# Optimization experiments

Measured on AMD Instinct MI355X. Metric: run time of the kernel, lower is better.

## Reference

```python
import jax, jax.numpy as jnp
import numpy as np

N_NODES = 50000
N_EDGES = 800000
IN_CH = 256
HID = 32
HEADS = 8
OUT_CH = 64
NEG_SLOPE = 0.2


def _glorot(key, shape):
    fan = shape[0] + shape[-1]
    lim = jnp.sqrt(6.0 / fan)
    return jax.random.uniform(key, shape, jnp.float32, -lim, lim)


def setup_inputs() -> dict:
    key = jax.random.key(0)
    ks = jax.random.split(key, 12)
    x = jax.random.normal(ks[0], (N_NODES, IN_CH), jnp.float32)
    edge_index = jax.random.randint(ks[1], (2, N_EDGES), 0, N_NODES, jnp.int64 if jax.config.jax_enable_x64 else jnp.int32)
    # conv1: in -> heads*hid, concat
    W1 = _glorot(ks[2], (IN_CH, HEADS * HID))
    a_src1 = _glorot(ks[3], (HEADS, HID))
    a_dst1 = _glorot(ks[4], (HEADS, HID))
    b1 = jnp.zeros((HEADS * HID,), jnp.float32)
    # conv2: heads*hid -> heads*hid, 1 head
    W2 = _glorot(ks[5], (HEADS * HID, HEADS * HID))
    a_src2 = _glorot(ks[6], (1, HEADS * HID))
    a_dst2 = _glorot(ks[7], (1, HEADS * HID))
    b2 = jnp.zeros((HEADS * HID,), jnp.float32)
    # final linear
    Wlin = _glorot(ks[8], (HEADS * HID, OUT_CH))
    blin = jnp.zeros((OUT_CH,), jnp.float32)
    return {"x": x, "edge_index": edge_index, "W1": W1, "a_src1": a_src1,
            "a_dst1": a_dst1, "b1": b1, "W2": W2, "a_src2": a_src2,
            "a_dst2": a_dst2, "b2": b2, "Wlin": Wlin, "blin": blin}


def gat_conv(x, src, dst, W, a_src, a_dst, bias, heads, out_ch):
    n = x.shape[0]
    h = (x @ W).reshape(n, heads, out_ch)            # [N, H, C]
    # per-node attention halves, then gather per edge (cheaper than edge-first)
    s = jnp.einsum('nhc,hc->nh', h, a_src)[src]      # [E, H]
    d = jnp.einsum('nhc,hc->nh', h, a_dst)[dst]      # [E, H]
    e = jax.nn.leaky_relu(s + d, NEG_SLOPE)          # [E, H]
    # segment softmax over incoming edges of each dst node
    emax = jax.ops.segment_max(e, dst, num_segments=n)
    e = jnp.exp(e - jax.lax.stop_gradient(emax)[dst])
    denom = jax.ops.segment_sum(e, dst, num_segments=n)
    alpha = e / denom[dst]                           # [E, H]
    msg = h[src] * alpha[:, :, None]                 # [E, H, C]
    out = jax.ops.segment_sum(msg, dst, num_segments=n)
    return out.reshape(n, heads * out_ch) + bias


def reference(x, edge_index, W1, a_src1, a_dst1, b1, W2, a_src2, a_dst2, b2, Wlin, blin):
    n = x.shape[0]
    # PyG GATConv adds self-loops by default
    loops = jnp.arange(n, dtype=edge_index.dtype)
    src = jnp.concatenate([edge_index[0], loops])
    dst = jnp.concatenate([edge_index[1], loops])
    # dropout (p=0.6) is identity in eval mode
    h = jax.nn.elu(gat_conv(x, src, dst, W1, a_src1, a_dst1, b1, HEADS, HID))
    h = jax.nn.elu(gat_conv(h, src, dst, W2, a_src2, a_dst2, b2, 1, HEADS * HID))
    return h @ Wlin + blin
```

## Files before the change

### kernel.cpp

```cpp
#include <hip/hip_runtime.h>
#include <hip/hip_bf16.h>
#include <hip/hip_fp16.h>

typedef __attribute__((ext_vector_type(8))) short short8;
typedef __attribute__((ext_vector_type(4))) float f32x4;

#define GLL(g, s) __builtin_amdgcn_global_load_lds(                        \
    (const __attribute__((address_space(1))) void*)(g),                    \
    (__attribute__((address_space(3))) void*)(s), 16, 0, 0)

__device__ __forceinline__ ushort f2bf(float f) {
    unsigned u = __float_as_uint(f);
    u += 0x7fffu + ((u >> 16) & 1u);
    return (ushort)(u >> 16);
}
__device__ __forceinline__ float bf2f(ushort h) {
    return __uint_as_float(((unsigned)h) << 16);
}
__device__ __forceinline__ float elu_f(float x) {
    return x > 0.0f ? x : expm1f(x);
}
__device__ __forceinline__ float lrelu(float x) {
    return x < 0.0f ? 0.2f * x : x;
}

__global__ void hist_kernel(const int* __restrict__ ei, int* __restrict__ deg, int E, int n) {
    int total = E + n;
    for (int i = blockIdx.x * blockDim.x + threadIdx.x; i < total; i += gridDim.x * blockDim.x) {
        int d = (i < E) ? ei[E + i] : (i - E);
        atomicAdd(&deg[d], 1);
    }
}

__global__ __launch_bounds__(256) void partial_kernel(const int* __restrict__ deg, int* __restrict__ bsums, int n) {
    __shared__ int sm[256];
    int t = threadIdx.x;
    int idx = blockIdx.x * 256 + t;
    sm[t] = (idx < n) ? deg[idx] : 0;
    __syncthreads();
    #pragma unroll
    for (int off = 128; off > 0; off >>= 1) {
        if (t < off) sm[t] += sm[t + off];
        __syncthreads();
    }
    if (t == 0) bsums[blockIdx.x] = sm[0];
}

__global__ __launch_bounds__(256) void scanblocks_kernel(const int* __restrict__ bsums, int* __restrict__ boff,
                                                         int* __restrict__ rowptr, int nb, int n) {
    __shared__ int sm[256];
    int t = threadIdx.x;
    int carry = 0;
    for (int base = 0; base < nb; base += 256) {
        int i = base + t;
        int v = (i < nb) ? bsums[i] : 0;
        sm[t] = v;
        __syncthreads();
        #pragma unroll
        for (int off = 1; off < 256; off <<= 1) {
            int x = (t >= off) ? sm[t - off] : 0;
            __syncthreads();
            sm[t] += x;
            __syncthreads();
        }
        if (i < nb) boff[i] = carry + sm[t] - v;
        int tot = sm[255];
        __syncthreads();
        carry += tot;
    }
    if (t == 0) rowptr[n] = carry;
}

__global__ __launch_bounds__(256) void finalize_kernel(const int* __restrict__ deg, const int* __restrict__ boff,
                                                       int* __restrict__ rowptr, int* __restrict__ cursor, int n) {
    __shared__ int sm[256];
    int t = threadIdx.x;
    int idx = blockIdx.x * 256 + t;
    int v = (idx < n) ? deg[idx] : 0;
    sm[t] = v;
    __syncthreads();
    #pragma unroll
    for (int off = 1; off < 256; off <<= 1) {
        int x = (t >= off) ? sm[t - off] : 0;
        __syncthreads();
        sm[t] += x;
        __syncthreads();
    }
    if (idx < n) {
        int ex = boff[blockIdx.x] + sm[t] - v;
        rowptr[idx] = ex;
        cursor[idx] = ex;
    }
}

__global__ void scatter_kernel(const int* __restrict__ ei, int* __restrict__ cursor,
                               int* __restrict__ csr_src, int E, int n) {
    int total = E + n;
    for (int i = blockIdx.x * blockDim.x + threadIdx.x; i < total; i += gridDim.x * blockDim.x) {
        int s, d;
        if (i < E) { s = ei[i]; d = ei[E + i]; }
        else       { s = i - E; d = s; }
        int pos = atomicAdd(&cursor[d], 1);
        csr_src[pos] = s;
    }
}

__global__ void wconv_kernel(const float* __restrict__ W, short* __restrict__ hi,
                             short* __restrict__ lo, int KN, int Ncols) {
    int idx = blockIdx.x * 256 + threadIdx.x;
    if (idx >= KN) return;
    int k = idx / Ncols, n = idx - k * Ncols;
    float v = W[idx];
    ushort h = f2bf(v);
    ushort l = f2bf(v - bf2f(h));
    size_t o = ((size_t)(k >> 3) * Ncols + n) * 8 + (k & 7);
    hi[o] = (short)h;
    lo[o] = (short)l;
}

template<int N, bool OUTHALF>
__global__ __launch_bounds__(256, 2) void gemm_mfma(const float* __restrict__ A,
                                                    const short* __restrict__ Bph,
                                                    const short* __restrict__ Bpl,
                                                    const float* __restrict__ bias,
                                                    void* __restrict__ Cout, int M) {
    constexpr int FN = (N == 256) ? 4 : 1;
    __shared__ short Bh[4][2][4][64][8];
    __shared__ short Bl[4][2][4][64][8];
    const int tid = threadIdx.x;
    const int lane = tid & 63;
    const int wave = tid >> 6;
    const int r0 = blockIdx.x * 64;
    const int c = lane >> 4;
    const int rs = lane & 15;
    const int c0 = (N == 256) ? wave * 64 : 0;
    const int colin = (N == 256) ? rs : (wave * 16 + rs);

    const float* aBase[4];
    #pragma unroll
    for (int fm = 0; fm < 4; ++fm) {
        int r = r0 + fm * 16 + rs;
        if (r > M - 1) r = M - 1;
        aBase[fm] = A + (size_t)r * 256 + c * 8;
    }

    float4 aregA[8], aregB[8];
    auto loadA = [&](float4* ar, int t) {
        #pragma unroll
        for (int fm = 0; fm < 4; ++fm) {
            ar[2 * fm]     = *(const float4*)(aBase[fm] + t * 32);
            ar[2 * fm + 1] = *(const float4*)(aBase[fm] + t * 32 + 4);
        }
    };
    auto issueB = [&](int buf, int t) {
        #pragma unroll
        for (int q = 0; q < 4; ++q) {
            const short* sh = Bph + ((size_t)(t * 4 + q) * N + c0 + lane) * 8;
            const short* sl = Bpl + ((size_t)(t * 4 + q) * N + c0 + lane) * 8;
            GLL(sh, &Bh[wave][buf][q][0][0]);
            GLL(sl, &Bl[wave][buf][q][0][0]);
        }
    };
    auto convA = [&](const float4* ar, short8* ah, short8* al) {
        #pragma unroll
        for (int fm = 0; fm < 4; ++fm) {
            float f[8] = {ar[2 * fm].x, ar[2 * fm].y, ar[2 * fm].z, ar[2 * fm].w,
                          ar[2 * fm + 1].x, ar[2 * fm + 1].y, ar[2 * fm + 1].z, ar[2 * fm + 1].w};
            short8 hi, lo;
            #pragma unroll
            for (int j = 0; j < 8; ++j) {
                ushort hb = f2bf(f[j]);
                hi[j] = (short)hb;
                lo[j] = (short)f2bf(f[j] - bf2f(hb));
            }
            ah[fm] = hi;
            al[fm] = lo;
        }
    };

    f32x4 acc[4][FN];
    #pragma unroll
    for (int i = 0; i < 4; ++i)
        #pragma unroll
        for (int j = 0; j < FN; ++j)
            acc[i][j] = (f32x4){0.f, 0.f, 0.f, 0.f};

    loadA(aregA, 0); issueB(0, 0);
    loadA(aregB, 1); issueB(1, 1);

    #pragma unroll
    for (int t = 0; t < 8; ++t) {
        if (t < 7) asm volatile("s_waitcnt vmcnt(16)" ::: "memory");
        else       asm volatile("s_waitcnt vmcnt(0)" ::: "memory");
        const int cur = t & 1;
        const float4* curA = (t & 1) ? aregB : aregA;
        short8 ah[4], al[4];
        convA(curA, ah, al);
        #pragma unroll
        for (int fn = 0; fn < FN; ++fn) {
            short8 bhv = *(const short8*)&Bh[wave][cur][c][colin + fn * 16][0];
            short8 blv = *(const short8*)&Bl[wave][cur][c][colin + fn * 16][0];
            #pragma unroll
            for (int fm = 0; fm < 4; ++fm) {
                acc[fm][fn] = __builtin_amdgcn_mfma_f32_16x16x32_bf16(ah[fm], bhv, acc[fm][fn], 0, 0, 0);
                acc[fm][fn] = __builtin_amdgcn_mfma_f32_16x16x32_bf16(ah[fm], blv, acc[fm][fn], 0, 0, 0);
                acc[fm][fn] = __builtin_amdgcn_mfma_f32_16x16x32_bf16(al[fm], bhv, acc[fm][fn], 0, 0, 0);
            }
        }
        asm volatile("s_waitcnt lgkmcnt(0)" ::: "memory");
        if (t < 6) {
            float4* nxtA = (t & 1) ? aregB : aregA;
            loadA(nxtA, t + 2);
            issueB(cur, t + 2);
        }
    }

    const int wn0 = wave * (N / 4);
    #pragma unroll
    for (int fn = 0; fn < FN; ++fn) {
        int col = wn0 + fn * 16 + rs;
        float bv = bias ? bias[col] : 0.0f;
        #pragma unroll
        for (int fm = 0; fm < 4; ++fm) {
            #pragma unroll
            for (int g = 0; g < 4; ++g) {
                int r = r0 + fm * 16 + c * 4 + g;
                if (r < M) {
                    float v = acc[fm][fn][g] + bv;
                    if constexpr (OUTHALF)
                        ((__half*)Cout)[(size_t)r * N + col] = __float2half_rn(v);
                    else
                        ((float*)Cout)[(size_t)r * N + col] = v;
                }
            }
        }
    }
}

template<int HEADS>
__global__ __launch_bounds__(256) void sd_kernel(const __half* __restrict__ h, const float* __restrict__ a_src,
                                                 const float* __restrict__ a_dst, float* __restrict__ s_out,
                                                 float* __restrict__ d_out_, int nnodes) {
    int lane = threadIdx.x & 63;
    int node = blockIdx.x * 4 + (threadIdx.x >> 6);
    if (node >= nnodes) return;
    const __half2* hp = (const __half2*)(h + (size_t)node * 256 + lane * 4);
    float2 f01 = __half22float2(hp[0]);
    float2 f23 = __half22float2(hp[1]);
    float4 as = *(const float4*)&a_src[lane * 4];
    float4 ad = *(const float4*)&a_dst[lane * 4];
    float ps = f01.x * as.x + f01.y * as.y + f23.x * as.z + f23.y * as.w;
    float pd = f01.x * ad.x + f01.y * ad.y + f23.x * ad.z + f23.y * ad.w;
    const int GS = 64 / HEADS;
    #pragma unroll
    for (int off = 1; off < GS; off <<= 1) {
        ps += __shfl_xor(ps, off);
        pd += __shfl_xor(pd, off);
    }
    int g = lane / GS;
    int r = lane & (GS - 1);
    if (r == 0) s_out[(size_t)node * HEADS + g] = ps;
    if (r == 1) d_out_[(size_t)node * HEADS + g] = pd;
}

template<int HEADS>
__global__ __launch_bounds__(256) void agg_kernel(const int* __restrict__ rowptr, const int* __restrict__ csr_src,
                                                  const __half* __restrict__ h, const float* __restrict__ s_att,
                                                  const float* __restrict__ d_att, const float* __restrict__ bias,
                                                  float* __restrict__ out, int nnodes) {
    int lane = threadIdx.x & 63;
    int node = blockIdx.x * 4 + (threadIdx.x >> 6);
    if (node >= nnodes) return;
    const int hh = (HEADS == 8) ? (lane >> 3) : 0;
    const int cbase = lane * 4;
    const int begin = rowptr[node], end = rowptr[node + 1];
    const float dl = d_att[(size_t)node * HEADS + hh];
    float m = -1e30f, den = 0.f;
    float ax = 0.f, ay = 0.f, az = 0.f, aw = 0.f;
    int i = begin;
    for (; i + 4 <= end; i += 4) {
        int s0 = csr_src[i], s1 = csr_src[i + 1], s2 = csr_src[i + 2], s3 = csr_src[i + 3];
        uint2 u0 = *(const uint2*)(h + (size_t)s0 * 256 + cbase);
        uint2 u1 = *(const uint2*)(h + (size_t)s1 * 256 + cbase);
        uint2 u2 = *(const uint2*)(h + (size_t)s2 * 256 + cbase);
        uint2 u3 = *(const uint2*)(h + (size_t)s3 * 256 + cbase);
        float v0 = lrelu(s_att[(size_t)s0 * HEADS + hh] + dl);
        float v1 = lrelu(s_att[(size_t)s1 * HEADS + hh] + dl);
        float v2 = lrelu(s_att[(size_t)s2 * HEADS + hh] + dl);
        float v3 = lrelu(s_att[(size_t)s3 * HEADS + hh] + dl);
        float vb = fmaxf(fmaxf(v0, v1), fmaxf(v2, v3));
        float mn = fmaxf(m, vb);
        float sc = __expf(m - mn);
        float w0 = __expf(v0 - mn), w1 = __expf(v1 - mn);
        float w2 = __expf(v2 - mn), w3 = __expf(v3 - mn);
        m = mn;
        den = den * sc + (w0 + w1) + (w2 + w3);
        float2 f0a = __half22float2(*(const __half2*)&u0.x), f0b = __half22float2(*(const __half2*)&u0.y);
        float2 f1a = __half22float2(*(const __half2*)&u1.x), f1b = __half22float2(*(const __half2*)&u1.y);
        float2 f2a = __half22float2(*(const __half2*)&u2.x), f2b = __half22float2(*(const __half2*)&u2.y);
        float2 f3a = __half22float2(*(const __half2*)&u3.x), f3b = __half22float2(*(const __half2*)&u3.y);
        ax = ax * sc + w0 * f0a.x + w1 * f1a.x + w2 * f2a.x + w3 * f3a.x;
        ay = ay * sc + w0 * f0a.y + w1 * f1a.y + w2 * f2a.y + w3 * f3a.y;
        az = az * sc + w0 * f0b.x + w1 * f1b.x + w2 * f2b.x + w3 * f3b.x;
        aw = aw * sc + w0 * f0b.y + w1 * f1b.y + w2 * f2b.y + w3 * f3b.y;
    }
    for (; i < end; ++i) {
        int s0 = csr_src[i];
        uint2 u0 = *(const uint2*)(h + (size_t)s0 * 256 + cbase);
        float v0 = lrelu(s_att[(size_t)s0 * HEADS + hh] + dl);
        float mn = fmaxf(m, v0);
        float sc = __expf(m - mn);
        float w0 = __expf(v0 - mn);
        m = mn;
        den = den * sc + w0;
        float2 f0a = __half22float2(*(const __half2*)&u0.x), f0b = __half22float2(*(const __half2*)&u0.y);
        ax = ax * sc + w0 * f0a.x;
        ay = ay * sc + w0 * f0a.y;
        az = az * sc + w0 * f0b.x;
        aw = aw * sc + w0 * f0b.y;
    }
    float inv = 1.0f / den;
    float4 bv = *(const float4*)&bias[cbase];
    float4 r;
    r.x = elu_f(ax * inv + bv.x);
    r.y = elu_f(ay * inv + bv.y);
    r.z = elu_f(az * inv + bv.z);
    r.w = elu_f(aw * inv + bv.w);
    *(float4*)&out[(size_t)node * 256 + cbase] = r;
}

extern "C" void kernel_launch(void* const* d_in, const int* in_sizes, int n_in,
                              void* d_out, int out_size, void* d_ws, size_t ws_size,
                              hipStream_t stream) {
    const float* x      = (const float*)d_in[0];
    const int*   ei     = (const int*)d_in[1];
    const float* W1     = (const float*)d_in[2];
    const float* a_src1 = (const float*)d_in[3];
    const float* a_dst1 = (const float*)d_in[4];
    const float* b1     = (const float*)d_in[5];
    const float* W2     = (const float*)d_in[6];
    const float* a_src2 = (const float*)d_in[7];
    const float* a_dst2 = (const float*)d_in[8];
    const float* b2     = (const float*)d_in[9];
    const float* Wlin   = (const float*)d_in[10];
    const float* blin   = (const float*)d_in[11];
    float* out = (float*)d_out;

    const int N = in_sizes[0] / 256;
    const int E = in_sizes[1] / 2;
    const int ET = E + N;
    const int NB = (N + 255) / 256;

    char* p = (char*)d_ws;
    auto alloc = [&](size_t bytes) {
        void* r = (void*)p;
        p += (bytes + 255) & ~size_t(255);
        return r;
    };
    __half* bufH  = (__half*)alloc((size_t)N * 256 * 2);
    float* bufB   = (float*)alloc((size_t)N * 256 * 4);
    float* s1     = (float*)alloc((size_t)N * 8 * 4);
    float* d1     = (float*)alloc((size_t)N * 8 * 4);
    float* s2     = (float*)alloc((size_t)N * 4);
    float* d2     = (float*)alloc((size_t)N * 4);
    int*   deg    = (int*)alloc((size_t)N * 4);
    int*   cursor = (int*)alloc((size_t)N * 4);
    int*   rowptr = (int*)alloc((size_t)(N + 1) * 4);
    int*   csr    = (int*)alloc((size_t)ET * 4);
    int*   bsums  = (int*)alloc((size_t)NB * 4);
    int*   boff   = (int*)alloc((size_t)NB * 4);
    short* W1h    = (short*)alloc((size_t)256 * 256 * 2);
    short* W1l    = (short*)alloc((size_t)256 * 256 * 2);
    short* W2h    = (short*)alloc((size_t)256 * 256 * 2);
    short* W2l    = (short*)alloc((size_t)256 * 256 * 2);
    short* W3h    = (short*)alloc((size_t)256 * 64 * 2);
    short* W3l    = (short*)alloc((size_t)256 * 64 * 2);

    hipMemsetAsync(deg, 0, (size_t)N * 4, stream);
    hist_kernel<<<(ET + 255) / 256, 256, 0, stream>>>(ei, deg, E, N);
    partial_kernel<<<NB, 256, 0, stream>>>(deg, bsums, N);
    scanblocks_kernel<<<1, 256, 0, stream>>>(bsums, boff, rowptr, NB, N);
    finalize_kernel<<<NB, 256, 0, stream>>>(deg, boff, rowptr, cursor, N);
    scatter_kernel<<<(ET + 255) / 256, 256, 0, stream>>>(ei, cursor, csr, E, N);

    wconv_kernel<<<(256 * 256 + 255) / 256, 256, 0, stream>>>(W1, W1h, W1l, 256 * 256, 256);
    wconv_kernel<<<(256 * 256 + 255) / 256, 256, 0, stream>>>(W2, W2h, W2l, 256 * 256, 256);
    wconv_kernel<<<(256 * 64 + 255) / 256, 256, 0, stream>>>(Wlin, W3h, W3l, 256 * 64, 64);

    const int gBlocks = (N + 63) / 64;
    const int nodeBlocks = (N + 3) / 4;

    gemm_mfma<256, true><<<gBlocks, 256, 0, stream>>>(x, W1h, W1l, nullptr, bufH, N);
    sd_kernel<8><<<nodeBlocks, 256, 0, stream>>>(bufH, a_src1, a_dst1, s1, d1, N);
    agg_kernel<8><<<nodeBlocks, 256, 0, stream>>>(rowptr, csr, bufH, s1, d1, b1, bufB, N);

    gemm_mfma<256, true><<<gBlocks, 256, 0, stream>>>(bufB, W2h, W2l, nullptr, bufH, N);
    sd_kernel<1><<<nodeBlocks, 256, 0, stream>>>(bufH, a_src2, a_dst2, s2, d2, N);
    agg_kernel<1><<<nodeBlocks, 256, 0, stream>>>(rowptr, csr, bufH, s2, d2, b2, bufB, N);

    gemm_mfma<64, false><<<gBlocks, 256, 0, stream>>>(bufB, W3h, W3l, blin, out, N);
}
```

Baseline: 517.4 us.

## Pre-pack activations to split-bf16, single-wave GEMMs, fixed-offset softmax, fused scan

The split-bf16 conversion of x moves into a single packing kernel, and the aggregation kernels now write their outputs straight into a k-major hi/lo bf16 layout. The GEMMs can then load A via global_load_lds instead of converting fp32 in registers. The GEMM becomes a 64-thread block with a 2D grid, and the scan's block-offset pass is merged into the finalize kernel. The aggregation drops the online-max softmax in favour of exp2 with a fixed offset of 30, which removes the rescaling work but risks overflow or underflow for attention logits far from that offset.

New measurement: 577.5 us. 11.6% more time.

```diff
diff --git a/kernel.cpp b/kernel.cpp
--- a/kernel.cpp
+++ b/kernel.cpp
@@ -46,36 +46,26 @@
     if (t == 0) bsums[blockIdx.x] = sm[0];
 }
 
-__global__ __launch_bounds__(256) void scanblocks_kernel(const int* __restrict__ bsums, int* __restrict__ boff,
-                                                         int* __restrict__ rowptr, int nb, int n) {
+__global__ __launch_bounds__(256) void finalize2_kernel(const int* __restrict__ deg, const int* __restrict__ bsums,
+                                                        int* __restrict__ rowptr, int* __restrict__ cursor,
+                                                        int n, int nb) {
     __shared__ int sm[256];
-    int t = threadIdx.x;
-    int carry = 0;
-    for (int base = 0; base < nb; base += 256) {
-        int i = base + t;
-        int v = (i < nb) ? bsums[i] : 0;
-        sm[t] = v;
+    __shared__ int sbase;
+    int t = threadIdx.x, b = blockIdx.x;
+    int part = 0;
+    for (int i = t; i < b; i += 256) part += bsums[i];
+    sm[t] = part;
+    __syncthreads();
+    #pragma unroll
+    for (int off = 128; off > 0; off >>= 1) {
+        if (t < off) sm[t] += sm[t + off];
         __syncthreads();
-        #pragma unroll
-        for (int off = 1; off < 256; off <<= 1) {
-            int x = (t >= off) ? sm[t - off] : 0;
-            __syncthreads();
-            sm[t] += x;
-            __syncthreads();
-        }
-        if (i < nb) boff[i] = carry + sm[t] - v;
-        int tot = sm[255];
-        __syncthreads();
-        carry += tot;
-    }
-    if (t == 0) rowptr[n] = carry;
-}
-
-__global__ __launch_bounds__(256) void finalize_kernel(const int* __restrict__ deg, const int* __restrict__ boff,
-                                                       int* __restrict__ rowptr, int* __restrict__ cursor, int n) {
-    __shared__ int sm[256];
-    int t = threadIdx.x;
-    int idx = blockIdx.x * 256 + t;
+    }
+    if (t == 0) sbase = sm[0];
+    __syncthreads();
+    int base = sbase;
+    __syncthreads();
+    int idx = b * 256 + t;
     int v = (idx < n) ? deg[idx] : 0;
     sm[t] = v;
     __syncthreads();
@@ -87,10 +77,11 @@
         __syncthreads();
     }
     if (idx < n) {
-        int ex = boff[blockIdx.x] + sm[t] - v;
+        int ex = base + sm[t] - v;
         rowptr[idx] = ex;
         cursor[idx] = ex;
     }
+    if (b == nb - 1 && t == 255) rowptr[n] = base + sm[255];
 }
 
 __global__ void scatter_kernel(const int* __restrict__ ei, int* __restrict__ cursor,
@@ -105,76 +96,73 @@
     }
 }
 
-__global__ void wconv_kernel(const float* __restrict__ W, short* __restrict__ hi,
-                             short* __restrict__ lo, int KN, int Ncols) {
-    int idx = blockIdx.x * 256 + threadIdx.x;
-    if (idx >= KN) return;
+__global__ __launch_bounds__(256) void packall_kernel(const float* __restrict__ x,
+                                                      const float* __restrict__ W1,
+                                                      const float* __restrict__ W2,
+                                                      const float* __restrict__ W3,
+                                                      short* __restrict__ xh, short* __restrict__ xl,
+                                                      short* __restrict__ w1h, short* __restrict__ w1l,
+                                                      short* __restrict__ w2h, short* __restrict__ w2l,
+                                                      short* __restrict__ w3h, short* __restrict__ w3l,
+                                                      int M, int Mpad, int XB) {
+    int b = blockIdx.x;
+    int t = threadIdx.x;
+    if (b < XB) {
+        int r = b * 8 + (t >> 5);
+        int cc = t & 31;
+        if (r >= M) return;
+        const float* src = x + (size_t)r * 256 + cc * 8;
+        short8 hi, lo;
+        #pragma unroll
+        for (int j = 0; j < 8; ++j) {
+            float v = src[j];
+            ushort h = f2bf(v);
+            hi[j] = (short)h;
+            lo[j] = (short)f2bf(v - bf2f(h));
+        }
+        size_t o = ((size_t)cc * Mpad + r) * 8;
+        *(short8*)(xh + o) = hi;
+        *(short8*)(xl + o) = lo;
+        return;
+    }
+    const float* W; short* hh; short* ll; int Ncols; int base;
+    if (b < XB + 256)      { W = W1; hh = w1h; ll = w1l; Ncols = 256; base = XB; }
+    else if (b < XB + 512) { W = W2; hh = w2h; ll = w2l; Ncols = 256; base = XB + 256; }
+    else                   { W = W3; hh = w3h; ll = w3l; Ncols = 64;  base = XB + 512; }
+    int idx = (b - base) * 256 + t;
     int k = idx / Ncols, n = idx - k * Ncols;
     float v = W[idx];
     ushort h = f2bf(v);
     ushort l = f2bf(v - bf2f(h));
     size_t o = ((size_t)(k >> 3) * Ncols + n) * 8 + (k & 7);
-    hi[o] = (short)h;
-    lo[o] = (short)l;
-}
-
-template<int N, bool OUTHALF>
-__global__ __launch_bounds__(256, 2) void gemm_mfma(const float* __restrict__ A,
-                                                    const short* __restrict__ Bph,
-                                                    const short* __restrict__ Bpl,
-                                                    const float* __restrict__ bias,
-                                                    void* __restrict__ Cout, int M) {
-    constexpr int FN = (N == 256) ? 4 : 1;
-    __shared__ short Bh[4][2][4][64][8];
-    __shared__ short Bl[4][2][4][64][8];
-    const int tid = threadIdx.x;
-    const int lane = tid & 63;
-    const int wave = tid >> 6;
+    hh[o] = (short)h;
+    ll[o] = (short)l;
+}
+
+template<int FN, bool OUTHALF>
+__global__ __launch_bounds__(64) void gemm_pk(const short* __restrict__ Aph, const short* __restrict__ Apl,
+                                              const short* __restrict__ Bph, const short* __restrict__ Bpl,
+                                              const float* __restrict__ bias, void* __restrict__ Cout,
+                                              int M, int Mpad, int NCOLS) {
+    __shared__ short Ah[2][4][64][8], Al[2][4][64][8];
+    __shared__ short Bh[2][4][FN * 16][8], Bl[2][4][FN * 16][8];
+    const int lane = threadIdx.x;
     const int r0 = blockIdx.x * 64;
+    const int c0 = blockIdx.y * FN * 16;
     const int c = lane >> 4;
     const int rs = lane & 15;
-    const int c0 = (N == 256) ? wave * 64 : 0;
-    const int colin = (N == 256) ? rs : (wave * 16 + rs);
-
-    const float* aBase[4];
-    #pragma unroll
-    for (int fm = 0; fm < 4; ++fm) {
-        int r = r0 + fm * 16 + rs;
-        if (r > M - 1) r = M - 1;
-        aBase[fm] = A + (size_t)r * 256 + c * 8;
-    }
-
-    float4 aregA[8], aregB[8];
-    auto loadA = [&](float4* ar, int t) {
-        #pragma unroll
-        for (int fm = 0; fm < 4; ++fm) {
-            ar[2 * fm]     = *(const float4*)(aBase[fm] + t * 32);
-            ar[2 * fm + 1] = *(const float4*)(aBase[fm] + t * 32 + 4);
-        }
-    };
-    auto issueB = [&](int buf, int t) {
+
+    auto issue = [&](int buf, int t) {
         #pragma unroll
         for (int q = 0; q < 4; ++q) {
-            const short* sh = Bph + ((size_t)(t * 4 + q) * N + c0 + lane) * 8;
-            const short* sl = Bpl + ((size_t)(t * 4 + q) * N + c0 + lane) * 8;
-            GLL(sh, &Bh[wave][buf][q][0][0]);
-            GLL(sl, &Bl[wave][buf][q][0][0]);
-        }
-    };
-    auto convA = [&](const float4* ar, short8* ah, short8* al) {
-        #pragma unroll
-        for (int fm = 0; fm < 4; ++fm) {
-            float f[8] = {ar[2 * fm].x, ar[2 * fm].y, ar[2 * fm].z, ar[2 * fm].w,
-                          ar[2 * fm + 1].x, ar[2 * fm + 1].y, ar[2 * fm + 1].z, ar[2 * fm + 1].w};
-            short8 hi, lo;
+            int kc = t * 4 + q;
+            GLL(Aph + ((size_t)kc * Mpad + r0 + lane) * 8, &Ah[buf][q][0][0]);
+            GLL(Apl + ((size_t)kc * Mpad + r0 + lane) * 8, &Al[buf][q][0][0]);
             #pragma unroll
-            for (int j = 0; j < 8; ++j) {
-                ushort hb = f2bf(f[j]);
-                hi[j] = (short)hb;
-                lo[j] = (short)f2bf(f[j] - bf2f(hb));
+            for (int hseg = 0; hseg < FN / 4; ++hseg) {
+                GLL(Bph + ((size_t)kc * NCOLS + c0 + hseg * 64 + lane) * 8, &Bh[buf][q][hseg * 64][0]);
+                GLL(Bpl + ((size_t)kc * NCOLS + c0 + hseg * 64 + lane) * 8, &Bl[buf][q][hseg * 64][0]);
             }
-            ah[fm] = hi;
-            al[fm] = lo;
         }
     };
 
@@ -185,40 +173,48 @@
         for (int j = 0; j < FN; ++j)
             acc[i][j] = (f32x4){0.f, 0.f, 0.f, 0.f};
 
-    loadA(aregA, 0); issueB(0, 0);
-    loadA(aregB, 1); issueB(1, 1);
+    issue(0, 0);
+    issue(1, 1);
 
     #pragma unroll
     for (int t = 0; t < 8; ++t) {
-        if (t < 7) asm volatile("s_waitcnt vmcnt(16)" ::: "memory");
-        else       asm volatile("s_waitcnt vmcnt(0)" ::: "memory");
-        const int cur = t & 1;
-        const float4* curA = (t & 1) ? aregB : aregA;
+        if (t < 7) {
+            if constexpr (FN == 8) asm volatile("s_waitcnt vmcnt(24)" ::: "memory");
+            else                   asm volatile("s_waitcnt vmcnt(16)" ::: "memory");
+        } else {
+            asm volatile("s_waitcnt vmcnt(0)" ::: "memory");
+        }
+        __builtin_amdgcn_sched_barrier(0);
+        const int buf = t & 1;
         short8 ah[4], al[4];
-        convA(curA, ah, al);
+        #pragma unroll
+        for (int fm = 0; fm < 4; ++fm) {
+            ah[fm] = *(const short8*)&Ah[buf][c][fm * 16 + rs][0];
+            al[fm] = *(const short8*)&Al[buf][c][fm * 16 + rs][0];
+        }
+        short8 bh[FN], bl[FN];
         #pragma unroll
         for (int fn = 0; fn < FN; ++fn) {
-            short8 bhv = *(const short8*)&Bh[wave][cur][c][colin + fn * 16][0];
-            short8 blv = *(const short8*)&Bl[wave][cur][c][colin + fn * 16][0];
+            bh[fn] = *(const short8*)&Bh[buf][c][fn * 16 + rs][0];
+            bl[fn] = *(const short8*)&Bl[buf][c][fn * 16 + rs][0];
+        }
+        asm volatile("s_waitcnt lgkmcnt(0)" ::: "memory");
+        __builtin_amdgcn_sched_barrier(0);
+        if (t < 6) issue(buf, t + 2);
+        #pragma unroll
+        for (int fn = 0; fn < FN; ++fn) {
             #pragma unroll
             for (int fm = 0; fm < 4; ++fm) {
-                acc[fm][fn] = __builtin_amdgcn_mfma_f32_16x16x32_bf16(ah[fm], bhv, acc[fm][fn], 0, 0, 0);
-                acc[fm][fn] = __builtin_amdgcn_mfma_f32_16x16x32_bf16(ah[fm], blv, acc[fm][fn], 0, 0, 0);
-                acc[fm][fn] = __builtin_amdgcn_mfma_f32_16x16x32_bf16(al[fm], bhv, acc[fm][fn], 0, 0, 0);
+                acc[fm][fn] = __builtin_amdgcn_mfma_f32_16x16x32_bf16(ah[fm], bh[fn], acc[fm][fn], 0, 0, 0);
+                acc[fm][fn] = __builtin_amdgcn_mfma_f32_16x16x32_bf16(ah[fm], bl[fn], acc[fm][fn], 0, 0, 0);
+                acc[fm][fn] = __builtin_amdgcn_mfma_f32_16x16x32_bf16(al[fm], bh[fn], acc[fm][fn], 0, 0, 0);
             }
         }
-        asm volatile("s_waitcnt lgkmcnt(0)" ::: "memory");
-        if (t < 6) {
-            float4* nxtA = (t & 1) ? aregB : aregA;
-            loadA(nxtA, t + 2);
-            issueB(cur, t + 2);
-        }
-    }
-
-    const int wn0 = wave * (N / 4);
+    }
+
     #pragma unroll
     for (int fn = 0; fn < FN; ++fn) {
-        int col = wn0 + fn * 16 + rs;
+        int col = c0 + fn * 16 + rs;
         float bv = bias ? bias[col] : 0.0f;
         #pragma unroll
         for (int fm = 0; fm < 4; ++fm) {
@@ -228,9 +224,9 @@
                 if (r < M) {
                     float v = acc[fm][fn][g] + bv;
                     if constexpr (OUTHALF)
-                        ((__half*)Cout)[(size_t)r * N + col] = __float2half_rn(v);
+                        ((__half*)Cout)[(size_t)r * NCOLS + col] = __float2half_rn(v);
                     else
-                        ((float*)Cout)[(size_t)r * N + col] = v;
+                        ((float*)Cout)[(size_t)r * NCOLS + col] = v;
                 }
             }
         }
@@ -259,15 +255,16 @@
     }
     int g = lane / GS;
     int r = lane & (GS - 1);
-    if (r == 0) s_out[(size_t)node * HEADS + g] = ps;
-    if (r == 1) d_out_[(size_t)node * HEADS + g] = pd;
+    if (r == 0) s_out[(size_t)node * HEADS + g] = ps * 1.44269504f;
+    if (r == 1) d_out_[(size_t)node * HEADS + g] = pd * 1.44269504f;
 }
 
 template<int HEADS>
 __global__ __launch_bounds__(256) void agg_kernel(const int* __restrict__ rowptr, const int* __restrict__ csr_src,
                                                   const __half* __restrict__ h, const float* __restrict__ s_att,
                                                   const float* __restrict__ d_att, const float* __restrict__ bias,
-                                                  float* __restrict__ out, int nnodes) {
+                                                  short* __restrict__ outh, short* __restrict__ outl,
+                                                  int nnodes, int Mpad) {
     int lane = threadIdx.x & 63;
     int node = blockIdx.x * 4 + (threadIdx.x >> 6);
     if (node >= nnodes) return;
@@ -275,7 +272,7 @@
     const int cbase = lane * 4;
     const int begin = rowptr[node], end = rowptr[node + 1];
     const float dl = d_att[(size_t)node * HEADS + hh];
-    float m = -1e30f, den = 0.f;
+    float den = 0.f;
     float ax = 0.f, ay = 0.f, az = 0.f, aw = 0.f;
     int i = begin;
     for (; i + 4 <= end; i += 4) {
@@ -284,49 +281,48 @@
         uint2 u1 = *(const uint2*)(h + (size_t)s1 * 256 + cbase);
         uint2 u2 = *(const uint2*)(h + (size_t)s2 * 256 + cbase);
         uint2 u3 = *(const uint2*)(h + (size_t)s3 * 256 + cbase);
-        float v0 = lrelu(s_att[(size_t)s0 * HEADS + hh] + dl);
-        float v1 = lrelu(s_att[(size_t)s1 * HEADS + hh] + dl);
-        float v2 = lrelu(s_att[(size_t)s2 * HEADS + hh] + dl);
-        float v3 = lrelu(s_att[(size_t)s3 * HEADS + hh] + dl);
-        float vb = fmaxf(fmaxf(v0, v1), fmaxf(v2, v3));
-        float mn = fmaxf(m, vb);
-        float sc = __expf(m - mn);
-        float w0 = __expf(v0 - mn), w1 = __expf(v1 - mn);
-        float w2 = __expf(v2 - mn), w3 = __expf(v3 - mn);
-        m = mn;
-        den = den * sc + (w0 + w1) + (w2 + w3);
+        float w0 = exp2f(lrelu(s_att[(size_t)s0 * HEADS + hh] + dl) - 30.0f);
+        float w1 = exp2f(lrelu(s_att[(size_t)s1 * HEADS + hh] + dl) - 30.0f);
+        float w2 = exp2f(lrelu(s_att[(size_t)s2 * HEADS + hh] + dl) - 30.0f);
+        float w3 = exp2f(lrelu(s_att[(size_t)s3 * HEADS + hh] + dl) - 30.0f);
+        den += (w0 + w1) + (w2 + w3);
         float2 f0a = __half22float2(*(const __half2*)&u0.x), f0b = __half22float2(*(const __half2*)&u0.y);
         float2 f1a = __half22float2(*(const __half2*)&u1.x), f1b = __half22float2(*(const __half2*)&u1.y);
         float2 f2a = __half22float2(*(const __half2*)&u2.x), f2b = __half22float2(*(const __half2*)&u2.y);
         float2 f3a = __half22float2(*(const __half2*)&u3.x), f3b = __half22float2(*(const __half2*)&u3.y);
-        ax = ax * sc + w0 * f0a.x + w1 * f1a.x + w2 * f2a.x + w3 * f3a.x;
-        ay = ay * sc + w0 * f0a.y + w1 * f1a.y + w2 * f2a.y + w3 * f3a.y;
-        az = az * sc + w0 * f0b.x + w1 * f1b.x + w2 * f2b.x + w3 * f3b.x;
-        aw = aw * sc + w0 * f0b.y + w1 * f1b.y + w2 * f2b.y + w3 * f3b.y;
+        ax += w0 * f0a.x + w1 * f1a.x + w2 * f2a.x + w3 * f3a.x;
+        ay += w0 * f0a.y + w1 * f1a.y + w2 * f2a.y + w3 * f3a.y;
+        az += w0 * f0b.x + w1 * f1b.x + w2 * f2b.x + w3 * f3b.x;
+        aw += w0 * f0b.y + w1 * f1b.y + w2 * f2b.y + w3 * f3b.y;
     }
     for (; i < end; ++i) {
         int s0 = csr_src[i];
         uint2 u0 = *(const uint2*)(h + (size_t)s0 * 256 + cbase);
-        float v0 = lrelu(s_att[(size_t)s0 * HEADS + hh] + dl);
-        float mn = fmaxf(m, v0);
-        float sc = __expf(m - mn);
-        float w0 = __expf(v0 - mn);
-        m = mn;
-        den = den * sc + w0;
+        float w0 = exp2f(lrelu(s_att[(size_t)s0 * HEADS + hh] + dl) - 30.0f);
+        den += w0;
         float2 f0a = __half22float2(*(const __half2*)&u0.x), f0b = __half22float2(*(const __half2*)&u0.y);
-        ax = ax * sc + w0 * f0a.x;
-        ay = ay * sc + w0 * f0a.y;
-        az = az * sc + w0 * f0b.x;
-        aw = aw * sc + w0 * f0b.y;
+        ax += w0 * f0a.x;
+        ay += w0 * f0a.y;
+        az += w0 * f0b.x;
+        aw += w0 * f0b.y;
     }
     float inv = 1.0f / den;
     float4 bv = *(const float4*)&bias[cbase];
-    float4 r;
-    r.x = elu_f(ax * inv + bv.x);
-    r.y = elu_f(ay * inv + bv.y);
-    r.z = elu_f(az * inv + bv.z);
-    r.w = elu_f(aw * inv + bv.w);
-    *(float4*)&out[(size_t)node * 256 + cbase] = r;
+    float r0 = elu_f(ax * inv + bv.x);
+    float r1 = elu_f(ay * inv + bv.y);
+    float r2 = elu_f(az * inv + bv.z);
+    float r3 = elu_f(aw * inv + bv.w);
+    ushort h0 = f2bf(r0), h1 = f2bf(r1), h2 = f2bf(r2), h3 = f2bf(r3);
+    ushort l0 = f2bf(r0 - bf2f(h0)), l1 = f2bf(r1 - bf2f(h1));
+    ushort l2 = f2bf(r2 - bf2f(h2)), l3 = f2bf(r3 - bf2f(h3));
+    size_t o = ((size_t)(lane >> 1) * Mpad + node) * 8 + (lane & 1) * 4;
+    uint2 hv, lv;
+    hv.x = (unsigned)h0 | ((unsigned)h1 << 16);
+    hv.y = (unsigned)h2 | ((unsigned)h3 << 16);
+    lv.x = (unsigned)l0 | ((unsigned)l1 << 16);
+    lv.y = (unsigned)l2 | ((unsigned)l3 << 16);
+    *(uint2*)(outh + o) = hv;
+    *(uint2*)(outl + o) = lv;
 }
 
 extern "C" void kernel_launch(void* const* d_in, const int* in_sizes, int n_in,
@@ -350,6 +346,7 @@
     const int E = in_sizes[1] / 2;
     const int ET = E + N;
     const int NB = (N + 255) / 256;
+    const int Mpad = ((N + 63) / 64) * 64;
 
     char* p = (char*)d_ws;
     auto alloc = [&](size_t bytes) {
@@ -358,7 +355,8 @@
         return r;
     };
     __half* bufH  = (__half*)alloc((size_t)N * 256 * 2);
-    float* bufB   = (float*)alloc((size_t)N * 256 * 4);
+    short* Aph    = (short*)alloc((size_t)Mpad * 256 * 2);
+    short* Apl    = (short*)alloc((size_t)Mpad * 256 * 2);
     float* s1     = (float*)alloc((size_t)N * 8 * 4);
     float* d1     = (float*)alloc((size_t)N * 8 * 4);
     float* s2     = (float*)alloc((size_t)N * 4);
@@ -368,7 +366,6 @@
     int*   rowptr = (int*)alloc((size_t)(N + 1) * 4);
     int*   csr    = (int*)alloc((size_t)ET * 4);
     int*   bsums  = (int*)alloc((size_t)NB * 4);
-    int*   boff   = (int*)alloc((size_t)NB * 4);
     short* W1h    = (short*)alloc((size_t)256 * 256 * 2);
     short* W1l    = (short*)alloc((size_t)256 * 256 * 2);
     short* W2h    = (short*)alloc((size_t)256 * 256 * 2);
@@ -379,24 +376,24 @@
     hipMemsetAsync(deg, 0, (size_t)N * 4, stream);
     hist_kernel<<<(ET + 255) / 256, 256, 0, stream>>>(ei, deg, E, N);
     partial_kernel<<<NB, 256, 0, stream>>>(deg, bsums, N);
-    scanblocks_kernel<<<1, 256, 0, stream>>>(bsums, boff, rowptr, NB, N);
-    finalize_kernel<<<NB, 256, 0, stream>>>(deg, boff, rowptr, cursor, N);
+    finalize2_kernel<<<NB, 256, 0, stream>>>(deg, bsums, rowptr, cursor, N, NB);
     scatter_kernel<<<(ET + 255) / 256, 256, 0, stream>>>(ei, cursor, csr, E, N);
 
-    wconv_kernel<<<(256 * 256 + 255) / 256, 256, 0, stream>>>(W1, W1h, W1l, 256 * 256, 256);
-    wconv_kernel<<<(256 * 256 + 255) / 256, 256, 0, stream>>>(W2, W2h, W2l, 256 * 256, 256);
-    wconv_kernel<<<(256 * 64 + 255) / 256, 256, 0, stream>>>(Wlin, W3h, W3l, 256 * 64, 64);
+    const int XB = (N + 7) / 8;
+    packall_kernel<<<XB + 512 + 64, 256, 0, stream>>>(x, W1, W2, Wlin,
+                                                      Aph, Apl, W1h, W1l, W2h, W2l, W3h, W3l,
+                                                      N, Mpad, XB);
 
     const int gBlocks = (N + 63) / 64;
     const int nodeBlocks = (N + 3) / 4;
 
-    gemm_mfma<256, true><<<gBlocks, 256, 0, stream>>>(x, W1h, W1l, nullptr, bufH, N);
+    gemm_pk<8, true><<<dim3(gBlocks, 2), 64, 0, stream>>>(Aph, Apl, W1h, W1l, nullptr, bufH, N, Mpad, 256);
     sd_kernel<8><<<nodeBlocks, 256, 0, stream>>>(bufH, a_src1, a_dst1, s1, d1, N);
-    agg_kernel<8><<<nodeBlocks, 256, 0, stream>>>(rowptr, csr, bufH, s1, d1, b1, bufB, N);
-
-    gemm_mfma<256, true><<<gBlocks, 256, 0, stream>>>(bufB, W2h, W2l, nullptr, bufH, N);
+    agg_kernel<8><<<nodeBlocks, 256, 0, stream>>>(rowptr, csr, bufH, s1, d1, b1, Aph, Apl, N, Mpad);
+
+    gemm_pk<8, true><<<dim3(gBlocks, 2), 64, 0, stream>>>(Aph, Apl, W2h, W2l, nullptr, bufH, N, Mpad, 256);
     sd_kernel<1><<<nodeBlocks, 256, 0, stream>>>(bufH, a_src2, a_dst2, s2, d2, N);
-    agg_kernel<1><<<nodeBlocks, 256, 0, stream>>>(rowptr, csr, bufH, s2, d2, b2, bufB, N);
-
-    gemm_mfma<64, false><<<gBlocks, 256, 0, stream>>>(bufB, W3h, W3l, blin, out, N);
-}
+    agg_kernel<1><<<nodeBlocks, 256, 0, stream>>>(rowptr, csr, bufH, s2, d2, b2, Aph, Apl, N, Mpad);
+
+    gemm_pk<4, false><<<dim3(gBlocks, 1), 64, 0, stream>>>(Aph, Apl, W3h, W3l, blin, out, N, Mpad, 64);
+}
```
